# Kernel optimization log

Measured on AMD Instinct MI355X. Metric: run time of the kernel, lower is better.

The kernel has to match this reference:

```python
import jax, jax.numpy as jnp
import numpy as np

V, D, B, NEG, L = 100000, 128, 4096, 5, 6


def setup_inputs() -> dict:
    key = jax.random.key(0)
    ks = jax.random.split(key, 8)
    initrange = 0.5 / D
    return {
        "u_emb": jax.random.uniform(ks[0], (V, D), jnp.float32, -initrange, initrange),
        "v_emb": jax.random.uniform(ks[1], (V, D), jnp.float32, -initrange, initrange),
        "pos_u_idx": jax.random.randint(ks[2], (B, L), 0, V),
        "pos_u_len": jax.random.randint(ks[3], (B,), 0, L),
        "pos_v_idx": jax.random.randint(ks[4], (B, L), 0, V),
        "pos_v_len": jax.random.randint(ks[5], (B,), 0, L),
        "neg_v_idx": jax.random.randint(ks[6], (B * NEG, L), 0, V),
        "neg_v_len": jax.random.randint(ks[7], (B * NEG,), 0, L),
    }


def _mean_pool(table, idx, length):
    # ragged phrase mean-pool: actual lengths are length+1 in [1, L]
    n = (length + 1).astype(jnp.int32)                      # [M]
    mask = (jnp.arange(L)[None, :] < n[:, None])            # [M, L]
    emb = table[idx]                                        # [M, L, D]
    summed = jnp.sum(emb * mask[:, :, None].astype(table.dtype), axis=1)
    return summed / n[:, None].astype(table.dtype)          # [M, D]


def reference(u_emb, v_emb, pos_u_idx, pos_u_len, pos_v_idx, pos_v_len, neg_v_idx, neg_v_len):
    embed_u = _mean_pool(u_emb, pos_u_idx, pos_u_len)       # [B, D]
    embed_v = _mean_pool(v_emb, pos_v_idx, pos_v_len)       # [B, D]
    neg_embed_v = _mean_pool(v_emb, neg_v_idx, neg_v_len).reshape(B, NEG, D)

    score = jnp.sum(embed_u * embed_v, axis=1)              # [B]
    log_target = jax.nn.log_sigmoid(score)                  # [B]
    neg_score = jnp.einsum("bnd,bd->bn", neg_embed_v, embed_u)  # [B, NEG]
    sum_log_sampled = jnp.sum(jax.nn.log_sigmoid(-neg_score), axis=1)
    loss = log_target + sum_log_sampled
    return -jnp.sum(loss) / float(B)
```

## Files before the change

### kernel.cpp

```cpp
#include <hip/hip_runtime.h>

#define V_SZ 100000
#define D_SZ 128
#define B_SZ 4096
#define NEG_SZ 5
#define L_SZ 6

__device__ __forceinline__ float log_sigmoid(float x) {
    float ax = fabsf(x);
    return fminf(x, 0.0f) - log1pf(__expf(-ax));
}

__device__ __forceinline__ float wave_reduce_sum(float v) {
    #pragma unroll
    for (int off = 32; off > 0; off >>= 1) v += __shfl_xor(v, off);
    return v;
}

template <bool ATOMIC>
__global__ __launch_bounds__(256) void skipgram_loss_kernel(
    const float* __restrict__ u_emb,
    const float* __restrict__ v_emb,
    const int* __restrict__ pos_u_idx,
    const int* __restrict__ pos_u_len,
    const int* __restrict__ pos_v_idx,
    const int* __restrict__ pos_v_len,
    const int* __restrict__ neg_v_idx,
    const int* __restrict__ neg_v_len,
    float* __restrict__ out)
{
    __shared__ float lds[7 * D_SZ];

    const int b    = blockIdx.x;
    const int wave = threadIdx.x >> 6;
    const int lane = threadIdx.x & 63;
    const int half = lane >> 5;
    const int dof  = (lane & 31) * 4;

    const int* idxp[2];
    const float* tab[2];
    int n[2], p[2];
    #pragma unroll
    for (int q = 0; q < 2; ++q) {
        const int pp = wave + 3 * q;
        p[q] = pp;
        if (pp == 0) {
            idxp[q] = pos_u_idx + b * L_SZ; tab[q] = u_emb; n[q] = pos_u_len[b] + 1;
        } else if (pp == 1) {
            idxp[q] = pos_v_idx + b * L_SZ; tab[q] = v_emb; n[q] = pos_v_len[b] + 1;
        } else {
            const int m = b * NEG_SZ + pp - 2;
            idxp[q] = neg_v_idx + m * L_SZ; tab[q] = v_emb; n[q] = neg_v_len[m] + 1;
        }
    }

    int id[2][L_SZ];
    #pragma unroll
    for (int q = 0; q < 2; ++q)
        #pragma unroll
        for (int l = 0; l < L_SZ; ++l) id[q][l] = idxp[q][l];

    float4 r[2][3];
    #pragma unroll
    for (int q = 0; q < 2; ++q)
        #pragma unroll
        for (int j = 0; j < 3; ++j) {
            const int idx = half ? id[q][2 * j + 1] : id[q][2 * j];
            r[q][j] = *reinterpret_cast<const float4*>(
                &tab[q][(size_t)idx * D_SZ + dof]);
        }

    #pragma unroll
    for (int q = 0; q < 2; ++q) {
        float4 a = make_float4(0.f, 0.f, 0.f, 0.f);
        #pragma unroll
        for (int j = 0; j < 3; ++j) {
            const bool valid = (2 * j + half) < n[q];
            a.x += valid ? r[q][j].x : 0.f;
            a.y += valid ? r[q][j].y : 0.f;
            a.z += valid ? r[q][j].z : 0.f;
            a.w += valid ? r[q][j].w : 0.f;
        }
        a.x += __shfl_xor(a.x, 32);
        a.y += __shfl_xor(a.y, 32);
        a.z += __shfl_xor(a.z, 32);
        a.w += __shfl_xor(a.w, 32);
        const float inv = 1.0f / (float)n[q];
        a.x *= inv; a.y *= inv; a.z *= inv; a.w *= inv;
        if (lane < 32)
            *reinterpret_cast<float4*>(&lds[p[q] * D_SZ + dof]) = a;
    }
    __syncthreads();

    if (wave == 0) {
        const float2 eu = *reinterpret_cast<const float2*>(&lds[0 * D_SZ + 2 * lane]);
        float s[6];
        #pragma unroll
        for (int k = 0; k < 6; ++k) {
            const float2 vp = *reinterpret_cast<const float2*>(
                &lds[(k + 1) * D_SZ + 2 * lane]);
            s[k] = eu.x * vp.x + eu.y * vp.y;
        }
        #pragma unroll
        for (int k = 0; k < 6; ++k) s[k] = wave_reduce_sum(s[k]);
        if (lane == 0) {
            float loss = log_sigmoid(s[0]);
            #pragma unroll
            for (int k = 1; k < 6; ++k) loss += log_sigmoid(-s[k]);
            if (ATOMIC) atomicAdd(out, -loss / (float)B_SZ);
            else        out[b] = loss;
        }
    }
}

__global__ __launch_bounds__(256) void skipgram_reduce_kernel(
    const float* __restrict__ per_b, float* __restrict__ out)
{
    __shared__ float s[4];
    float acc = 0.0f;
    for (int i = threadIdx.x; i < B_SZ; i += 256) acc += per_b[i];
    acc = wave_reduce_sum(acc);
    const int wave = threadIdx.x >> 6;
    const int lane = threadIdx.x & 63;
    if (lane == 0) s[wave] = acc;
    __syncthreads();
    if (threadIdx.x == 0) {
        out[0] = -(s[0] + s[1] + s[2] + s[3]) / (float)B_SZ;
    }
}

extern "C" void kernel_launch(void* const* d_in, const int* in_sizes, int n_in,
                              void* d_out, int out_size, void* d_ws, size_t ws_size,
                              hipStream_t stream) {
    const float* u_emb     = (const float*)d_in[0];
    const float* v_emb     = (const float*)d_in[1];
    const int*   pos_u_idx = (const int*)d_in[2];
    const int*   pos_u_len = (const int*)d_in[3];
    const int*   pos_v_idx = (const int*)d_in[4];
    const int*   pos_v_len = (const int*)d_in[5];
    const int*   neg_v_idx = (const int*)d_in[6];
    const int*   neg_v_len = (const int*)d_in[7];
    float* out = (float*)d_out;

    if (ws_size >= (size_t)B_SZ * sizeof(float)) {
        float* per_b = (float*)d_ws;
        skipgram_loss_kernel<false><<<B_SZ, 256, 0, stream>>>(
            u_emb, v_emb, pos_u_idx, pos_u_len, pos_v_idx, pos_v_len,
            neg_v_idx, neg_v_len, per_b);
        skipgram_reduce_kernel<<<1, 256, 0, stream>>>(per_b, out);
    } else {
        hipMemsetAsync(d_out, 0, sizeof(float), stream);
        skipgram_loss_kernel<true><<<B_SZ, 256, 0, stream>>>(
            u_emb, v_emb, pos_u_idx, pos_u_len, pos_v_idx, pos_v_len,
            neg_v_idx, neg_v_len, out);
    }
}
```

Before: 27.92 us.

## Process two batch rows per block and make index loads scalar

Each 256-thread block now handles two batch rows, with every wave pooling four phrases and the last slot padded with a duplicate negative. This halves the grid to amortise per-block overhead and keeps waves fully busy. Index and length loads are made wave-uniform with readfirstlane so they can go through scalar loads. log1pf is replaced with the faster __logf, and the reduce kernel reads float4. The fallback path for a small workspace is removed, so the code now assumes the workspace is always large enough.

```diff
diff --git a/kernel.cpp b/kernel.cpp
--- a/kernel.cpp
+++ b/kernel.cpp
@@ -7,8 +7,7 @@
 #define L_SZ 6
 
 __device__ __forceinline__ float log_sigmoid(float x) {
-    float ax = fabsf(x);
-    return fminf(x, 0.0f) - log1pf(__expf(-ax));
+    return fminf(x, 0.0f) - __logf(1.0f + __expf(-fabsf(x)));
 }
 
 __device__ __forceinline__ float wave_reduce_sum(float v) {
@@ -17,7 +16,6 @@
     return v;
 }
 
-template <bool ATOMIC>
 __global__ __launch_bounds__(256) void skipgram_loss_kernel(
     const float* __restrict__ u_emb,
     const float* __restrict__ v_emb,
@@ -27,42 +25,47 @@
     const int* __restrict__ pos_v_len,
     const int* __restrict__ neg_v_idx,
     const int* __restrict__ neg_v_len,
-    float* __restrict__ out)
+    float* __restrict__ per_b)
 {
-    __shared__ float lds[7 * D_SZ];
+    __shared__ float lds[2][8][D_SZ];
 
-    const int b    = blockIdx.x;
+    const int b0   = blockIdx.x * 2;
     const int wave = threadIdx.x >> 6;
     const int lane = threadIdx.x & 63;
     const int half = lane >> 5;
     const int dof  = (lane & 31) * 4;
 
-    const int* idxp[2];
-    const float* tab[2];
-    int n[2], p[2];
+    const int* idxp[4];
+    const float* tab[4];
+    int n[4], sb[4], sp[4];
     #pragma unroll
-    for (int q = 0; q < 2; ++q) {
-        const int pp = wave + 3 * q;
-        p[q] = pp;
-        if (pp == 0) {
+    for (int q = 0; q < 4; ++q) {
+        const int bb = q >> 1;
+        const int pp = wave + 4 * (q & 1);
+        const int b  = b0 + bb;
+        const int eff = (pp == 7) ? 3 : pp;
+        sb[q] = bb; sp[q] = pp;
+        if (eff == 0) {
             idxp[q] = pos_u_idx + b * L_SZ; tab[q] = u_emb; n[q] = pos_u_len[b] + 1;
-        } else if (pp == 1) {
+        } else if (eff == 1) {
             idxp[q] = pos_v_idx + b * L_SZ; tab[q] = v_emb; n[q] = pos_v_len[b] + 1;
         } else {
-            const int m = b * NEG_SZ + pp - 2;
+            const int m = b * NEG_SZ + (eff - 2);
             idxp[q] = neg_v_idx + m * L_SZ; tab[q] = v_emb; n[q] = neg_v_len[m] + 1;
         }
+        n[q] = __builtin_amdgcn_readfirstlane(n[q]);
     }
 
-    int id[2][L_SZ];
+    int id[4][L_SZ];
     #pragma unroll
-    for (int q = 0; q < 2; ++q)
+    for (int q = 0; q < 4; ++q)
         #pragma unroll
-        for (int l = 0; l < L_SZ; ++l) id[q][l] = idxp[q][l];
+        for (int l = 0; l < L_SZ; ++l)
+            id[q][l] = __builtin_amdgcn_readfirstlane(idxp[q][l]);
 
-    float4 r[2][3];
+    float4 r[4][3];
     #pragma unroll
-    for (int q = 0; q < 2; ++q)
+    for (int q = 0; q < 4; ++q)
         #pragma unroll
         for (int j = 0; j < 3; ++j) {
             const int idx = half ? id[q][2 * j + 1] : id[q][2 * j];
@@ -71,7 +74,7 @@
         }
 
     #pragma unroll
-    for (int q = 0; q < 2; ++q) {
+    for (int q = 0; q < 4; ++q) {
         float4 a = make_float4(0.f, 0.f, 0.f, 0.f);
         #pragma unroll
         for (int j = 0; j < 3; ++j) {
@@ -88,17 +91,17 @@
         const float inv = 1.0f / (float)n[q];
         a.x *= inv; a.y *= inv; a.z *= inv; a.w *= inv;
         if (lane < 32)
-            *reinterpret_cast<float4*>(&lds[p[q] * D_SZ + dof]) = a;
+            *reinterpret_cast<float4*>(&lds[sb[q]][sp[q]][dof]) = a;
     }
     __syncthreads();
 
-    if (wave == 0) {
-        const float2 eu = *reinterpret_cast<const float2*>(&lds[0 * D_SZ + 2 * lane]);
+    if (wave < 2) {
+        const float2 eu = *reinterpret_cast<const float2*>(&lds[wave][0][2 * lane]);
         float s[6];
         #pragma unroll
         for (int k = 0; k < 6; ++k) {
             const float2 vp = *reinterpret_cast<const float2*>(
-                &lds[(k + 1) * D_SZ + 2 * lane]);
+                &lds[wave][k + 1][2 * lane]);
             s[k] = eu.x * vp.x + eu.y * vp.y;
         }
         #pragma unroll
@@ -107,8 +110,7 @@
             float loss = log_sigmoid(s[0]);
             #pragma unroll
             for (int k = 1; k < 6; ++k) loss += log_sigmoid(-s[k]);
-            if (ATOMIC) atomicAdd(out, -loss / (float)B_SZ);
-            else        out[b] = loss;
+            per_b[b0 + wave] = loss;
         }
     }
 }
@@ -118,7 +120,12 @@
 {
     __shared__ float s[4];
     float acc = 0.0f;
-    for (int i = threadIdx.x; i < B_SZ; i += 256) acc += per_b[i];
+    #pragma unroll
+    for (int i = 0; i < 4; ++i) {
+        const float4 v = reinterpret_cast<const float4*>(per_b)[
+            i * 256 + threadIdx.x];
+        acc += (v.x + v.y) + (v.z + v.w);
+    }
     acc = wave_reduce_sum(acc);
     const int wave = threadIdx.x >> 6;
     const int lane = threadIdx.x & 63;
@@ -142,16 +149,9 @@
     const int*   neg_v_len = (const int*)d_in[7];
     float* out = (float*)d_out;
 
-    if (ws_size >= (size_t)B_SZ * sizeof(float)) {
-        float* per_b = (float*)d_ws;
-        skipgram_loss_kernel<false><<<B_SZ, 256, 0, stream>>>(
-            u_emb, v_emb, pos_u_idx, pos_u_len, pos_v_idx, pos_v_len,
-            neg_v_idx, neg_v_len, per_b);
-        skipgram_reduce_kernel<<<1, 256, 0, stream>>>(per_b, out);
-    } else {
-        hipMemsetAsync(d_out, 0, sizeof(float), stream);
-        skipgram_loss_kernel<true><<<B_SZ, 256, 0, stream>>>(
-            u_emb, v_emb, pos_u_idx, pos_u_len, pos_v_idx, pos_v_len,
-            neg_v_idx, neg_v_len, out);
-    }
+    float* per_b = (float*)d_ws;
+    skipgram_loss_kernel<<<B_SZ / 2, 256, 0, stream>>>(
+        u_emb, v_emb, pos_u_idx, pos_u_len, pos_v_idx, pos_v_len,
+        neg_v_idx, neg_v_len, per_b);
+    skipgram_reduce_kernel<<<1, 256, 0, stream>>>(per_b, out);
 }
```

Result: faster. 22.43 us (median of 2 runs) (-19.7%).
